# Kernel tuning notes

Measured on AMD Instinct MI355X. Metric: run time of the kernel, lower is better.

## Reference

```python
import jax, jax.numpy as jnp
import numpy as np

# 8 corner offsets of the trilinear cell: (8, 3)
_OFFS = jnp.array([[i, j, k] for i in (0, 1) for j in (0, 1) for k in (0, 1)], dtype=jnp.int32)


def _gridding(cloud, R):
    """Trilinear scatter of points into an RxRxR occupancy-weight grid.

    cloud: (b, n, 3) with coords in [-0.5, 0.5] (already divided by scale).
    Returns (b, R, R, R) grid where each point adds trilinear weights to its
    8 neighboring cells (the GRNet gridding_distance forward kernel).
    """
    b, n, _ = cloud.shape
    v = (cloud + 0.5) * R                      # continuous voxel coords in [0, R)
    lower = jnp.floor(v)
    frac = v - lower                           # (b, n, 3) in [0, 1)
    lower = lower.astype(jnp.int32)
    nb = lower[:, :, None, :] + _OFFS[None, None]              # (b, n, 8, 3)
    # per-axis trilinear weight: (1 - frac) for the low corner, frac for the high
    w_d = jnp.where(_OFFS[None, None] == 0,
                    1.0 - frac[:, :, None, :], frac[:, :, None, :])  # (b, n, 8, 3)
    w = jnp.prod(w_d, axis=-1)                                  # (b, n, 8)
    valid = jnp.all((nb >= 0) & (nb < R), axis=-1)              # (b, n, 8)
    w = jnp.where(valid, w, 0.0)
    nbc = jnp.clip(nb, 0, R - 1)
    flat = (nbc[..., 0] * R + nbc[..., 1]) * R + nbc[..., 2]    # (b, n, 8)
    batch_off = jnp.arange(b, dtype=jnp.int32)[:, None, None] * (R * R * R)
    idx = (flat + batch_off).reshape(-1)
    grid = jnp.zeros((b * R * R * R,), cloud.dtype).at[idx].add(w.reshape(-1))
    return grid.reshape(b, R, R, R)


def setup_inputs() -> dict:
    key = jax.random.key(0)
    k1, k2 = jax.random.split(key)
    R = 128
    B, N1, N2 = 16, 65536, 65536
    # coords in [-(R-2)/2, (R-2)/2] so that after /scale they are inside (-0.5, 0.5)
    pred = (jax.random.uniform(k1, (B, N1, 3), jnp.float32) - 0.5) * (R - 2)
    gt = (jax.random.uniform(k2, (B, N2, 3), jnp.float32) - 0.5) * (R - 2)
    return {"pred_cloud": pred, "gt_cloud": gt, "scale": R}


def reference(pred_cloud, gt_cloud, scale):
    pred = pred_cloud / scale
    gt = gt_cloud / scale
    return _gridding(pred, scale), _gridding(gt, scale)
```

## Files before the change

kernel.cpp:

```cpp
#include <hip/hip_runtime.h>
#include <stdint.h>


constexpr int R    = 128;
constexpr int R3c  = R * R * R;
constexpr int BPG  = 256;
constexpr int NBLK = 256;
constexpr int BLKT = 1024;
constexpr int NCH  = 8;
constexpr int MAXBINS = 8192;

constexpr size_t WS_HIST = 0;
constexpr size_t WS_CS   = 8u << 20;
constexpr size_t WS_TOT  = 9u << 20;
constexpr size_t WS_BASE = 10u << 20;
constexpr size_t WS_REC  = 16u << 20;

__device__ __forceinline__ void quant_point(float px, float py, float pz,
                                            uint32_t& xq, uint32_t& yq, uint32_t& zq)
{
    const float inv = 1.0f / 128.0f;
    const float S = 16384.0f;
    const uint32_t QMAX = (126u << 14) | 16383u;
    float vx = (px * inv + 0.5f) * 128.0f;
    float vy = (py * inv + 0.5f) * 128.0f;
    float vz = (pz * inv + 0.5f) * 128.0f;
    xq = min(__float2uint_rn(fmaxf(vx, 0.0f) * S), QMAX);
    yq = min(__float2uint_rn(fmaxf(vy, 0.0f) * S), QMAX);
    zq = min(__float2uint_rn(fmaxf(vz, 0.0f) * S), QMAX);
}

__device__ __forceinline__ uint2 pack_rec(uint32_t xq, uint32_t yq, uint32_t zq) {
    return make_uint2(xq | (yq << 21), (yq >> 11) | (zq << 10));
}
__device__ __forceinline__ void unpack_rec(uint2 r, uint32_t& xq, uint32_t& yq, uint32_t& zq) {
    xq = r.x & 0x1FFFFFu;
    yq = (r.x >> 21) | ((r.y & 0x3FFu) << 11);
    zq = (r.y >> 10) & 0x1FFFFFu;
}

__device__ __forceinline__ void load_point(
    const float* __restrict__ pred, const float* __restrict__ gt,
    int i, int total1, int n1, int n2, int B,
    float& px, float& py, float& pz, int& cb)
{
    const float* p;
    if (i < total1) { p = pred + (size_t)i * 3; cb = i / n1; }
    else { int j = i - total1; p = gt + (size_t)j * 3; cb = B + j / n2; }
    px = p[0]; py = p[1]; pz = p[2];
}

__device__ __forceinline__ void region_range(uint32_t xq, uint32_t yq, uint32_t zq,
                                             int& rx0, int& rx1, int& ry0, int& ry1,
                                             int& rz0, int& rz1)
{
    int ix = xq >> 14, iy = yq >> 14, iz = zq >> 14;
    rx0 = ix >> 4; rx1 = (ix + 1) >> 4;
    ry0 = iy >> 4; ry1 = (iy + 1) >> 4;
    rz0 = iz >> 5; rz1 = (iz + 1) >> 5;
}

__global__ __launch_bounds__(BLKT) void bin_hist(
    const float* __restrict__ pred, const float* __restrict__ gt,
    int total1, int P, int n1, int n2, int B, int ppb,
    uint16_t* __restrict__ hist, int NBINS)
{
    __shared__ uint32_t h[MAXBINS];
    for (int j = threadIdx.x; j < NBINS; j += BLKT) h[j] = 0;
    __syncthreads();

    int s = blockIdx.x * ppb, e = min(s + ppb, P);
    for (int i = s + threadIdx.x; i < e; i += BLKT) {
        float px, py, pz; int cb;
        load_point(pred, gt, i, total1, n1, n2, B, px, py, pz, cb);
        uint32_t xq, yq, zq;
        quant_point(px, py, pz, xq, yq, zq);
        int rx0, rx1, ry0, ry1, rz0, rz1;
        region_range(xq, yq, zq, rx0, rx1, ry0, ry1, rz0, rz1);
        int base = cb * BPG;
        for (int a = rx0; a <= rx1; ++a)
            for (int b = ry0; b <= ry1; ++b)
                for (int c = rz0; c <= rz1; ++c)
                    atomicAdd(&h[base + (a << 5) + (b << 2) + c], 1u);
    }
    __syncthreads();
    uint16_t* o = hist + (size_t)blockIdx.x * NBINS;
    for (int j = threadIdx.x; j < NBINS; j += BLKT) o[j] = (uint16_t)h[j];
}

__global__ __launch_bounds__(256) void scan_chunk(
    const uint16_t* __restrict__ hist, uint32_t* __restrict__ cs, int NBINS)
{
    int tid = blockIdx.x * 256 + threadIdx.x;
    if (tid >= NCH * NBINS) return;
    int c = tid / NBINS, j = tid - c * NBINS;
    int b0 = c * (NBLK / NCH);
    uint32_t s = 0;
    for (int b = b0; b < b0 + NBLK / NCH; ++b)
        s += hist[(size_t)b * NBINS + j];
    cs[c * NBINS + j] = s;
}

__global__ __launch_bounds__(256) void scan_fin(
    uint16_t* __restrict__ hist, const uint32_t* __restrict__ cs,
    uint32_t* __restrict__ tot, int NBINS)
{
    int tid = blockIdx.x * 256 + threadIdx.x;
    if (tid >= NCH * NBINS) return;
    int c = tid / NBINS, j = tid - c * NBINS;
    uint32_t run = 0;
    for (int cc = 0; cc < c; ++cc) run += cs[cc * NBINS + j];
    int b0 = c * (NBLK / NCH);
    for (int b = b0; b < b0 + NBLK / NCH; ++b) {
        size_t k = (size_t)b * NBINS + j;
        uint32_t t = hist[k];
        hist[k] = (uint16_t)run;
        run += t;
    }
    if (c == NCH - 1) tot[j] = run;
}

__global__ __launch_bounds__(256) void scan_base(
    const uint32_t* __restrict__ tot, uint32_t* __restrict__ base, int NBINS)
{
    __shared__ uint32_t part[256];
    int t = threadIdx.x;
    int chunk = NBINS / 256;
    uint32_t s = 0;
    for (int i = 0; i < chunk; ++i) s += tot[t * chunk + i];
    part[t] = s;
    __syncthreads();
    if (t == 0) {
        uint32_t run = 0;
        for (int i = 0; i < 256; ++i) { uint32_t v = part[i]; part[i] = run; run += v; }
    }
    __syncthreads();
    uint32_t run = part[t];
    for (int i = 0; i < chunk; ++i) {
        base[t * chunk + i] = run;
        run += tot[t * chunk + i];
    }
    if (t == 255) base[NBINS] = run;
}

__global__ __launch_bounds__(BLKT) void bin_scatter(
    const float* __restrict__ pred, const float* __restrict__ gt,
    int total1, int P, int n1, int n2, int B, int ppb,
    const uint16_t* __restrict__ hist, const uint32_t* __restrict__ base,
    uint2* __restrict__ records, int NBINS)
{
    __shared__ uint32_t cur[MAXBINS];
    const uint16_t* hrow = hist + (size_t)blockIdx.x * NBINS;
    for (int j = threadIdx.x; j < NBINS; j += BLKT)
        cur[j] = base[j] + (uint32_t)hrow[j];
    __syncthreads();

    int s = blockIdx.x * ppb, e = min(s + ppb, P);
    for (int i = s + threadIdx.x; i < e; i += BLKT) {
        float px, py, pz; int cb;
        load_point(pred, gt, i, total1, n1, n2, B, px, py, pz, cb);
        uint32_t xq, yq, zq;
        quant_point(px, py, pz, xq, yq, zq);
        int rx0, rx1, ry0, ry1, rz0, rz1;
        region_range(xq, yq, zq, rx0, rx1, ry0, ry1, rz0, rz1);
        int bb = cb * BPG;
        uint2 rec = pack_rec(xq, yq, zq);
        for (int a = rx0; a <= rx1; ++a)
            for (int b = ry0; b <= ry1; ++b)
                for (int c = rz0; c <= rz1; ++c) {
                    uint32_t slot = atomicAdd(&cur[bb + (a << 5) + (b << 2) + c], 1u);
                    records[slot] = rec;
                }
    }
}

__global__ __launch_bounds__(256) void accum_kernel(
    const uint32_t* __restrict__ base, const uint2* __restrict__ records,
    float* __restrict__ out)
{
    __shared__ float tile[16 * 16 * 32];
    int bin = blockIdx.x;
    int cb = bin >> 8;
    int region = bin & 255;
    int rx = region >> 5, ry = (region >> 2) & 7, rz = region & 3;

    float4* t4 = (float4*)tile;
    for (int t = threadIdx.x; t < 2048; t += 256)
        t4[t] = make_float4(0.f, 0.f, 0.f, 0.f);
    __syncthreads();

    uint32_t s = base[bin], e = base[bin + 1];
    const float FQ = 6.103515625e-05f;
    for (uint32_t r = s + threadIdx.x; r < e; r += 256) {
        uint32_t xq, yq, zq;
        unpack_rec(records[r], xq, yq, zq);
        int ix = xq >> 14, iy = yq >> 14, iz = zq >> 14;
        float fx = (float)(xq & 16383u) * FQ;
        float fy = (float)(yq & 16383u) * FQ;
        float fz = (float)(zq & 16383u) * FQ;
        float wx[2] = {1.0f - fx, fx};
        float wy[2] = {1.0f - fy, fy};
        float wz[2] = {1.0f - fz, fz};
        #pragma unroll
        for (int dx = 0; dx < 2; ++dx) {
            int cx = ix + dx;
            if ((cx >> 4) != rx) continue;
            #pragma unroll
            for (int dy = 0; dy < 2; ++dy) {
                int cy = iy + dy;
                if ((cy >> 4) != ry) continue;
                float wxy = wx[dx] * wy[dy];
                #pragma unroll
                for (int dz = 0; dz < 2; ++dz) {
                    int cz = iz + dz;
                    if ((cz >> 5) != rz) continue;
                    atomicAdd(&tile[(((cx & 15) << 4) + (cy & 15)) * 32 + (cz & 31)],
                              wxy * wz[dz]);
                }
            }
        }
    }
    __syncthreads();

    float* gout = out + (size_t)cb * R3c;
    for (int w = threadIdx.x; w < 2048; w += 256) {
        int lin = w * 4;
        int lx = lin >> 9, rem = lin & 511, ly = rem >> 5, lz = rem & 31;
        int X = rx * 16 + lx, Y = ry * 16 + ly, Z = rz * 32 + lz;
        *(float4*)&gout[((size_t)X * R + Y) * R + Z] = t4[w];
    }
}

__device__ __forceinline__ void point_math_f(float px, float py, float pz,
                                             int& ix, int& iy, int& iz,
                                             float& fx, float& fy, float& fz)
{
    const float inv = 1.0f / 128.0f;
    float vx = (px * inv + 0.5f) * 128.0f;
    float vy = (py * inv + 0.5f) * 128.0f;
    float vz = (pz * inv + 0.5f) * 128.0f;
    float lx = floorf(vx), ly = floorf(vy), lz = floorf(vz);
    fx = vx - lx; fy = vy - ly; fz = vz - lz;
    ix = min(max((int)lx, 0), R - 2);
    iy = min(max((int)ly, 0), R - 2);
    iz = min(max((int)lz, 0), R - 2);
}

__global__ __launch_bounds__(256) void gridding_scatter(
    const float* __restrict__ cloud, float* __restrict__ grid,
    int total_pts, int n_per_batch)
{
    int idx = blockIdx.x * blockDim.x + threadIdx.x;
    if (idx >= total_pts) return;
    int b = idx / n_per_batch;
    const float* p = cloud + (size_t)idx * 3;
    int ix, iy, iz; float fx, fy, fz;
    point_math_f(p[0], p[1], p[2], ix, iy, iz, fx, fy, fz);
    float wx[2] = {1.0f - fx, fx};
    float wy[2] = {1.0f - fy, fy};
    float wz[2] = {1.0f - fz, fz};
    float* gb = grid + (size_t)b * R3c;
    #pragma unroll
    for (int dx = 0; dx < 2; ++dx)
        #pragma unroll
        for (int dy = 0; dy < 2; ++dy) {
            float wxy = wx[dx] * wy[dy];
            #pragma unroll
            for (int dz = 0; dz < 2; ++dz)
                atomicAdd(gb + ((size_t)(ix + dx) * R + (iy + dy)) * R + (iz + dz),
                          wxy * wz[dz]);
        }
}

extern "C" void kernel_launch(void* const* d_in, const int* in_sizes, int n_in,
                              void* d_out, int out_size, void* d_ws, size_t ws_size,
                              hipStream_t stream) {
    const float* pred = (const float*)d_in[0];
    const float* gt   = (const float*)d_in[1];
    float* out = (float*)d_out;

    int total1 = in_sizes[0] / 3;
    int total2 = in_sizes[1] / 3;
    int B  = out_size / (2 * R3c);
    int n1 = total1 / B;
    int n2 = total2 / B;
    int NBINS = 2 * B * BPG;
    int P  = total1 + total2;
    int ppb = (P + NBLK - 1) / NBLK;

    size_t ws_need = WS_REC + (size_t)8 * P * 8;
    if (ws_size < ws_need || NBINS > MAXBINS || NBINS % 256 != 0) {
        hipMemsetAsync(d_out, 0, (size_t)out_size * sizeof(float), stream);
        gridding_scatter<<<(total1 + 255) / 256, 256, 0, stream>>>(pred, out, total1, n1);
        gridding_scatter<<<(total2 + 255) / 256, 256, 0, stream>>>(
            gt, out + (size_t)B * R3c, total2, n2);
        return;
    }

    uint16_t* hist  = (uint16_t*)((char*)d_ws + WS_HIST);
    uint32_t* cs    = (uint32_t*)((char*)d_ws + WS_CS);
    uint32_t* tot   = (uint32_t*)((char*)d_ws + WS_TOT);
    uint32_t* basep = (uint32_t*)((char*)d_ws + WS_BASE);
    uint2*    recs  = (uint2*)((char*)d_ws + WS_REC);

    int scan_thr = NCH * NBINS;

    bin_hist<<<NBLK, BLKT, 0, stream>>>(pred, gt, total1, P, n1, n2, B, ppb,
                                        hist, NBINS);
    scan_chunk<<<(scan_thr + 255) / 256, 256, 0, stream>>>(hist, cs, NBINS);
    scan_fin<<<(scan_thr + 255) / 256, 256, 0, stream>>>(hist, cs, tot, NBINS);
    scan_base<<<1, 256, 0, stream>>>(tot, basep, NBINS);
    bin_scatter<<<NBLK, BLKT, 0, stream>>>(pred, gt, total1, P, n1, n2, B, ppb,
                                           hist, basep, recs, NBINS);
    accum_kernel<<<NBINS, 256, 0, stream>>>(basep, recs, out);
}
```

Measured before the change: 388.6 us.

## Cache quantized point records from histogram pass and vectorize point loads

The histogram pass now loads points four at a time with float4 reads, quantizes them, and writes packed 8-byte records to a workspace buffer. The scatter pass reads those records instead of reloading and requantizing the float inputs. The change also doubles the block count while halving threads per block, adds an occupancy hint, and uses nontemporal stores for the output grid. The aim is less input traffic and arithmetic in the scatter pass, at the cost of an extra record buffer write and read and more histogram rows to scan.

```diff
diff --git a/kernel.cpp b/kernel.cpp
--- a/kernel.cpp
+++ b/kernel.cpp
@@ -5,29 +5,25 @@
 constexpr int R    = 128;
 constexpr int R3c  = R * R * R;
 constexpr int BPG  = 256;
-constexpr int NBLK = 256;
-constexpr int BLKT = 1024;
+constexpr int NBLK = 512;
+constexpr int BLKT = 512;
 constexpr int NCH  = 8;
 constexpr int MAXBINS = 8192;
 
 constexpr size_t WS_HIST = 0;
-constexpr size_t WS_CS   = 8u << 20;
-constexpr size_t WS_TOT  = 9u << 20;
-constexpr size_t WS_BASE = 10u << 20;
-constexpr size_t WS_REC  = 16u << 20;
-
-__device__ __forceinline__ void quant_point(float px, float py, float pz,
-                                            uint32_t& xq, uint32_t& yq, uint32_t& zq)
-{
-    const float inv = 1.0f / 128.0f;
+constexpr size_t WS_CS   = 16u << 20;
+constexpr size_t WS_TOT  = 17u << 20;
+constexpr size_t WS_BASE = 18u << 20;
+constexpr size_t WS_QREC = 20u << 20;
+constexpr size_t WS_REC  = 40u << 20;
+
+typedef float f4v __attribute__((ext_vector_type(4)));
+
+__device__ __forceinline__ uint32_t quant1(float p) {
     const float S = 16384.0f;
     const uint32_t QMAX = (126u << 14) | 16383u;
-    float vx = (px * inv + 0.5f) * 128.0f;
-    float vy = (py * inv + 0.5f) * 128.0f;
-    float vz = (pz * inv + 0.5f) * 128.0f;
-    xq = min(__float2uint_rn(fmaxf(vx, 0.0f) * S), QMAX);
-    yq = min(__float2uint_rn(fmaxf(vy, 0.0f) * S), QMAX);
-    zq = min(__float2uint_rn(fmaxf(vz, 0.0f) * S), QMAX);
+    float v = p + 64.0f;
+    return min(__float2uint_rn(fmaxf(v, 0.0f) * S), QMAX);
 }
 
 __device__ __forceinline__ uint2 pack_rec(uint32_t xq, uint32_t yq, uint32_t zq) {
@@ -60,28 +56,64 @@
     rz0 = iz >> 5; rz1 = (iz + 1) >> 5;
 }
 
-__global__ __launch_bounds__(BLKT) void bin_hist(
+__global__ __launch_bounds__(BLKT, 2) void bin_hist_qrec(
     const float* __restrict__ pred, const float* __restrict__ gt,
-    int total1, int P, int n1, int n2, int B, int ppb,
-    uint16_t* __restrict__ hist, int NBINS)
+    int total1, int P, int n1, int n2, int B, int ppb, int vec4ok,
+    uint16_t* __restrict__ hist, uint2* __restrict__ qrec, int NBINS)
 {
     __shared__ uint32_t h[MAXBINS];
     for (int j = threadIdx.x; j < NBINS; j += BLKT) h[j] = 0;
     __syncthreads();
 
     int s = blockIdx.x * ppb, e = min(s + ppb, P);
-    for (int i = s + threadIdx.x; i < e; i += BLKT) {
-        float px, py, pz; int cb;
-        load_point(pred, gt, i, total1, n1, n2, B, px, py, pz, cb);
-        uint32_t xq, yq, zq;
-        quant_point(px, py, pz, xq, yq, zq);
-        int rx0, rx1, ry0, ry1, rz0, rz1;
-        region_range(xq, yq, zq, rx0, rx1, ry0, ry1, rz0, rz1);
-        int base = cb * BPG;
-        for (int a = rx0; a <= rx1; ++a)
-            for (int b = ry0; b <= ry1; ++b)
-                for (int c = rz0; c <= rz1; ++c)
-                    atomicAdd(&h[base + (a << 5) + (b << 2) + c], 1u);
+    if (vec4ok) {
+        bool isgt = (s >= total1);
+        const float* src = isgt ? gt + (size_t)(s - total1) * 3
+                                : pred + (size_t)s * 3;
+        const int n = isgt ? n2 : n1;
+        const int cb0 = isgt ? B : 0;
+        const int loff = isgt ? total1 : 0;
+        const float4* src4 = (const float4*)src;
+        int ngrp = (e - s) >> 2;
+        for (int g = threadIdx.x; g < ngrp; g += BLKT) {
+            float4 a = src4[g * 3 + 0];
+            float4 b4 = src4[g * 3 + 1];
+            float4 c4 = src4[g * 3 + 2];
+            int li = (s + g * 4) - loff;
+            int hbase = (cb0 + li / n) * BPG;
+            float xs[4] = {a.x, a.w, b4.z, c4.y};
+            float ys[4] = {a.y, b4.x, b4.w, c4.z};
+            float zs[4] = {a.z, b4.y, c4.x, c4.w};
+            uint2 rec[4];
+            #pragma unroll
+            for (int q = 0; q < 4; ++q) {
+                uint32_t xq = quant1(xs[q]), yq = quant1(ys[q]), zq = quant1(zs[q]);
+                rec[q] = pack_rec(xq, yq, zq);
+                int rx0, rx1, ry0, ry1, rz0, rz1;
+                region_range(xq, yq, zq, rx0, rx1, ry0, ry1, rz0, rz1);
+                for (int aa = rx0; aa <= rx1; ++aa)
+                    for (int bb = ry0; bb <= ry1; ++bb)
+                        for (int cc = rz0; cc <= rz1; ++cc)
+                            atomicAdd(&h[hbase + (aa << 5) + (bb << 2) + cc], 1u);
+            }
+            uint4* q4 = (uint4*)(qrec + (size_t)s + (size_t)g * 4);
+            q4[0] = make_uint4(rec[0].x, rec[0].y, rec[1].x, rec[1].y);
+            q4[1] = make_uint4(rec[2].x, rec[2].y, rec[3].x, rec[3].y);
+        }
+    } else {
+        for (int i = s + threadIdx.x; i < e; i += BLKT) {
+            float px, py, pz; int cb;
+            load_point(pred, gt, i, total1, n1, n2, B, px, py, pz, cb);
+            uint32_t xq = quant1(px), yq = quant1(py), zq = quant1(pz);
+            qrec[i] = pack_rec(xq, yq, zq);
+            int rx0, rx1, ry0, ry1, rz0, rz1;
+            region_range(xq, yq, zq, rx0, rx1, ry0, ry1, rz0, rz1);
+            int base = cb * BPG;
+            for (int a = rx0; a <= rx1; ++a)
+                for (int b = ry0; b <= ry1; ++b)
+                    for (int c = rz0; c <= rz1; ++c)
+                        atomicAdd(&h[base + (a << 5) + (b << 2) + c], 1u);
+        }
     }
     __syncthreads();
     uint16_t* o = hist + (size_t)blockIdx.x * NBINS;
@@ -143,9 +175,9 @@
     if (t == 255) base[NBINS] = run;
 }
 
-__global__ __launch_bounds__(BLKT) void bin_scatter(
-    const float* __restrict__ pred, const float* __restrict__ gt,
-    int total1, int P, int n1, int n2, int B, int ppb,
+__global__ __launch_bounds__(BLKT, 2) void bin_scatter_qrec(
+    const uint2* __restrict__ qrec,
+    int total1, int P, int n1, int n2, int B, int ppb, int vec4ok,
     const uint16_t* __restrict__ hist, const uint32_t* __restrict__ base,
     uint2* __restrict__ records, int NBINS)
 {
@@ -156,21 +188,53 @@
     __syncthreads();
 
     int s = blockIdx.x * ppb, e = min(s + ppb, P);
-    for (int i = s + threadIdx.x; i < e; i += BLKT) {
-        float px, py, pz; int cb;
-        load_point(pred, gt, i, total1, n1, n2, B, px, py, pz, cb);
-        uint32_t xq, yq, zq;
-        quant_point(px, py, pz, xq, yq, zq);
-        int rx0, rx1, ry0, ry1, rz0, rz1;
-        region_range(xq, yq, zq, rx0, rx1, ry0, ry1, rz0, rz1);
-        int bb = cb * BPG;
-        uint2 rec = pack_rec(xq, yq, zq);
-        for (int a = rx0; a <= rx1; ++a)
-            for (int b = ry0; b <= ry1; ++b)
-                for (int c = rz0; c <= rz1; ++c) {
-                    uint32_t slot = atomicAdd(&cur[bb + (a << 5) + (b << 2) + c], 1u);
-                    records[slot] = rec;
-                }
+    if (vec4ok) {
+        bool isgt = (s >= total1);
+        const int n = isgt ? n2 : n1;
+        const int cb0 = isgt ? B : 0;
+        const int loff = isgt ? total1 : 0;
+        const uint4* qr4 = (const uint4*)(qrec + (size_t)s);
+        int ngrp = (e - s) >> 2;
+        for (int g = threadIdx.x; g < ngrp; g += BLKT) {
+            uint4 q0 = qr4[2 * g];
+            uint4 q1 = qr4[2 * g + 1];
+            uint2 rec[4] = {make_uint2(q0.x, q0.y), make_uint2(q0.z, q0.w),
+                            make_uint2(q1.x, q1.y), make_uint2(q1.z, q1.w)};
+            int li = (s + g * 4) - loff;
+            int bb = (cb0 + li / n) * BPG;
+            #pragma unroll
+            for (int q = 0; q < 4; ++q) {
+                uint32_t xq, yq, zq;
+                unpack_rec(rec[q], xq, yq, zq);
+                int rx0, rx1, ry0, ry1, rz0, rz1;
+                region_range(xq, yq, zq, rx0, rx1, ry0, ry1, rz0, rz1);
+                for (int aa = rx0; aa <= rx1; ++aa)
+                    for (int b2 = ry0; b2 <= ry1; ++b2)
+                        for (int cc = rz0; cc <= rz1; ++cc) {
+                            uint32_t slot =
+                                atomicAdd(&cur[bb + (aa << 5) + (b2 << 2) + cc], 1u);
+                            records[slot] = rec[q];
+                        }
+            }
+        }
+    } else {
+        for (int i = s + threadIdx.x; i < e; i += BLKT) {
+            int cb;
+            if (i < total1) cb = i / n1;
+            else            cb = B + (i - total1) / n2;
+            uint2 rec = qrec[i];
+            uint32_t xq, yq, zq;
+            unpack_rec(rec, xq, yq, zq);
+            int rx0, rx1, ry0, ry1, rz0, rz1;
+            region_range(xq, yq, zq, rx0, rx1, ry0, ry1, rz0, rz1);
+            int bb = cb * BPG;
+            for (int a = rx0; a <= rx1; ++a)
+                for (int b = ry0; b <= ry1; ++b)
+                    for (int c = rz0; c <= rz1; ++c) {
+                        uint32_t slot = atomicAdd(&cur[bb + (a << 5) + (b << 2) + c], 1u);
+                        records[slot] = rec;
+                    }
+        }
     }
 }
 
@@ -227,7 +291,8 @@
         int lin = w * 4;
         int lx = lin >> 9, rem = lin & 511, ly = rem >> 5, lz = rem & 31;
         int X = rx * 16 + lx, Y = ry * 16 + ly, Z = rz * 32 + lz;
-        *(float4*)&gout[((size_t)X * R + Y) * R + Z] = t4[w];
+        f4v v = ((const f4v*)tile)[w];
+        __builtin_nontemporal_store(v, (f4v*)&gout[((size_t)X * R + Y) * R + Z]);
     }
 }
 
@@ -297,20 +362,24 @@
         return;
     }
 
+    int vec4ok = (ppb % 4 == 0) && (total1 % ppb == 0) && (P % ppb == 0) &&
+                 (n1 % 4 == 0) && (n2 % 4 == 0);
+
     uint16_t* hist  = (uint16_t*)((char*)d_ws + WS_HIST);
     uint32_t* cs    = (uint32_t*)((char*)d_ws + WS_CS);
     uint32_t* tot   = (uint32_t*)((char*)d_ws + WS_TOT);
     uint32_t* basep = (uint32_t*)((char*)d_ws + WS_BASE);
+    uint2*    qrec  = (uint2*)((char*)d_ws + WS_QREC);
     uint2*    recs  = (uint2*)((char*)d_ws + WS_REC);
 
     int scan_thr = NCH * NBINS;
 
-    bin_hist<<<NBLK, BLKT, 0, stream>>>(pred, gt, total1, P, n1, n2, B, ppb,
-                                        hist, NBINS);
+    bin_hist_qrec<<<NBLK, BLKT, 0, stream>>>(pred, gt, total1, P, n1, n2, B, ppb,
+                                             vec4ok, hist, qrec, NBINS);
     scan_chunk<<<(scan_thr + 255) / 256, 256, 0, stream>>>(hist, cs, NBINS);
     scan_fin<<<(scan_thr + 255) / 256, 256, 0, stream>>>(hist, cs, tot, NBINS);
     scan_base<<<1, 256, 0, stream>>>(tot, basep, NBINS);
-    bin_scatter<<<NBLK, BLKT, 0, stream>>>(pred, gt, total1, P, n1, n2, B, ppb,
-                                           hist, basep, recs, NBINS);
+    bin_scatter_qrec<<<NBLK, BLKT, 0, stream>>>(qrec, total1, P, n1, n2, B, ppb,
+                                                vec4ok, hist, basep, recs, NBINS);
     accum_kernel<<<NBINS, 256, 0, stream>>>(basep, recs, out);
 }
```

Result: no change. 392.6 us (+1.0%).
